# Kernel optimization log

Measured on AMD Instinct MI355X. Metric: run time of the kernel, lower is better.

The kernel has to match this reference:

```python
import jax, jax.numpy as jnp
import numpy as np

N_NODES = 50000
N_EDGES = 600000
IN_CH = 128
OUT_CH = 128


def setup_inputs() -> dict:
    key = jax.random.key(0)
    k1, k2, k3, k4 = jax.random.split(key, 4)
    x = jax.random.normal(k1, (N_NODES, IN_CH), dtype=jnp.float32)
    edge_index = jax.random.randint(k2, (2, N_EDGES), 0, N_NODES, dtype=jnp.int64)
    W_msg = jax.random.normal(k3, (OUT_CH, IN_CH * 9), dtype=jnp.float32) * (1.0 / np.sqrt(IN_CH * 9))
    b_msg = jnp.zeros((OUT_CH,), dtype=jnp.float32)
    W_root = jax.random.normal(k4, (OUT_CH, IN_CH), dtype=jnp.float32) * (1.0 / np.sqrt(IN_CH))
    b_root = jnp.zeros((OUT_CH,), dtype=jnp.float32)
    return {"x": x, "edge_index": edge_index, "W_msg": W_msg, "b_msg": b_msg,
            "W_root": W_root, "b_root": b_root}


def reference(x, edge_index, W_msg, b_msg, W_root, b_root):
    n = x.shape[0]
    src = edge_index[0]
    dst = edge_index[1]

    # in-degree per destination node
    degree = jax.ops.segment_sum(jnp.ones_like(dst, dtype=x.dtype), dst, num_segments=n)  # [N]

    msgs = x[src]  # [E, C] gathered source features
    agg_sum = jax.ops.segment_sum(msgs, dst, num_segments=n)                 # [N, C]
    agg_mean = agg_sum / jnp.maximum(degree, 1.0)[:, None]                    # [N, C]
    agg_max = jax.ops.segment_max(msgs, dst, num_segments=n)                  # [N, C], -inf for empty
    agg_max = jnp.where(degree[:, None] > 0, agg_max, 0.0)

    degree_term = jnp.log1p(degree + 1.0)[:, None]                            # [N, 1]
    degree_reference = jnp.maximum(jnp.mean(jnp.log1p(degree + 1.0)), 1.0)    # scalar

    amp = degree_term / degree_reference                                       # [N, 1]
    att = degree_reference / jnp.maximum(degree_term, 1e-06)                   # [N, 1]

    feats = []
    for agg in (agg_sum, agg_mean, agg_max):
        feats.append(agg)            # identity
        feats.append(agg * amp)      # amplification
        feats.append(agg * att)      # attenuation
    stacked = jnp.concatenate(feats, axis=-1)                                  # [N, 9C]

    return stacked @ W_msg.T + b_msg + x @ W_root.T + b_root
```

## Files before the change

### kernel.cpp

```cpp
#include <hip/hip_runtime.h>
#include <cmath>

#define IN_CH 128
#define OUT_CH 128
#define KDIM 512
#define NGEMM 384
#define GBM 256
#define GBN 192
#define SLOT_B 40960
#define SLOT_US 20480
#define PIPE_LDS_BYTES (3 * SLOT_B)

typedef __attribute__((ext_vector_type(8))) short bfrag;
typedef __attribute__((ext_vector_type(4))) float f32x4;

__device__ __forceinline__ unsigned short f2bf(float f) {
    unsigned int u = __float_as_uint(f);
    return (unsigned short)((u + 0x7FFFu + ((u >> 16) & 1u)) >> 16);
}
__device__ __forceinline__ float bf2f(unsigned short h) {
    return __uint_as_float(((unsigned int)h) << 16);
}
__device__ __forceinline__ float4 unpack4(uint2 u) {
    float4 r;
    r.x = __uint_as_float(u.x << 16);
    r.y = __uint_as_float(u.x & 0xFFFF0000u);
    r.z = __uint_as_float(u.y << 16);
    r.w = __uint_as_float(u.y & 0xFFFF0000u);
    return r;
}

__device__ __forceinline__ void gl2lds16(const void* g, void* l) {
    __builtin_amdgcn_global_load_lds(
        (const __attribute__((address_space(1))) unsigned int*)g,
        (__attribute__((address_space(3))) unsigned int*)l, 16, 0, 0);
}


__global__ __launch_bounds__(256) void prep_kernel(const int* __restrict__ ei,
                                                   int* __restrict__ degree,
                                                   float* __restrict__ logsum,
                                                   const float* __restrict__ x,
                                                   unsigned short* __restrict__ xb,
                                                   int E, int total4) {
    int i = blockIdx.x * 256 + threadIdx.x;
    if (i == 0) logsum[0] = 0.f;
    if (i < E) atomicAdd(&degree[ei[E + i]], 1);
    if (i < total4) {
        float4 v = ((const float4*)x)[i];
        uint2 p;
        p.x = (unsigned)f2bf(v.x) | ((unsigned)f2bf(v.y) << 16);
        p.y = (unsigned)f2bf(v.z) | ((unsigned)f2bf(v.w) << 16);
        ((uint2*)xb)[i] = p;
    }
}

__global__ __launch_bounds__(256) void scan1_kernel(const int* __restrict__ degree,
                                                    int* __restrict__ part,
                                                    float* __restrict__ logsum, int n) {
    int i = blockIdx.x * 256 + threadIdx.x;
    int d = (i < n) ? degree[i] : 0;
    float lg = (i < n) ? logf((float)d + 2.0f) : 0.f;
    #pragma unroll
    for (int off = 32; off; off >>= 1) {
        d += __shfl_down(d, off);
        lg += __shfl_down(lg, off);
    }
    __shared__ int sd[4];
    __shared__ float sl[4];
    int wv = threadIdx.x >> 6;
    if ((threadIdx.x & 63) == 0) { sd[wv] = d; sl[wv] = lg; }
    __syncthreads();
    if (threadIdx.x == 0) {
        part[blockIdx.x] = (sd[0] + sd[1]) + (sd[2] + sd[3]);
        atomicAdd(&logsum[0], (sl[0] + sl[1]) + (sl[2] + sl[3]));
    }
}

__global__ __launch_bounds__(256) void scan3_kernel(const int* __restrict__ degree,
                                                    const int* __restrict__ part,
                                                    int* __restrict__ offsets,
                                                    int n, int E, int Sb) {
    int tid = threadIdx.x;
    int i = blockIdx.x * 256 + tid;
    int b = blockIdx.x;
    int acc0 = 0;
    for (int j = tid; j < b; j += 256) acc0 += part[j];
    #pragma unroll
    for (int off = 32; off; off >>= 1) acc0 += __shfl_down(acc0, off);
    __shared__ int bsum[4];
    int lane = tid & 63, wv = tid >> 6;
    if (lane == 0) bsum[wv] = acc0;
    __syncthreads();
    int base = (bsum[0] + bsum[1]) + (bsum[2] + bsum[3]);

    int d = (i < n) ? degree[i] : 0;
    int s = d;
    #pragma unroll
    for (int off = 1; off < 64; off <<= 1) {
        int t = __shfl_up(s, off);
        if (lane >= off) s += t;
    }
    __shared__ int wsum[4];
    if (lane == 63) wsum[wv] = s;
    __syncthreads();
    for (int w2 = 0; w2 < wv; ++w2) base += wsum[w2];
    if (i < n) offsets[i] = base + s - d;
    if (i == n - 1) offsets[n] = E;
}

__global__ void fill_kernel(const int* __restrict__ ei, int* __restrict__ offsets,
                            int* __restrict__ csr_src, int E) {
    int e = blockIdx.x * blockDim.x + threadIdx.x;
    if (e < E) {
        int src = ei[e];
        int dst = ei[E + e];
        int pos = atomicAdd(&offsets[dst], 1);
        csr_src[pos] = src;
    }
}


__global__ __launch_bounds__(256) void agg_kernel(const unsigned short* __restrict__ xb,
                                                  const int* __restrict__ csr_src,
                                                  const int* __restrict__ offsets,
                                                  const int* __restrict__ degree,
                                                  const float* __restrict__ logsum,
                                                  unsigned short* __restrict__ Zhi,
                                                  float* __restrict__ ampv,
                                                  float* __restrict__ attv,
                                                  int N, int Mpad) {
    int node = (blockIdx.x * 256 + threadIdx.x) >> 6;
    int lane = threadIdx.x & 63;
    if (node >= Mpad) return;
    int h = lane >> 5;
    int c4 = lane & 31;
    long zbase = (long)node * KDIM + c4 * 4;
    if (node >= N) {
        if (h == 0) {
            uint2 z = make_uint2(0u, 0u);
            #pragma unroll
            for (int sec = 0; sec < 4; ++sec) *(uint2*)&Zhi[zbase + sec * 128] = z;
        }
        return;
    }
    int deg = degree[node];
    int end = offsets[node];
    int beg = end - deg;
    const float NEG = -3.402823466e38f;
    float4 s[4], m[4];
    #pragma unroll
    for (int u = 0; u < 4; ++u) {
        s[u] = make_float4(0.f, 0.f, 0.f, 0.f);
        m[u] = make_float4(NEG, NEG, NEG, NEG);
    }
    int i = beg;
    for (; i + 8 <= end; i += 8) {
        int idx[4];
        #pragma unroll
        for (int u = 0; u < 4; ++u) idx[u] = csr_src[i + u * 2 + h];
        uint2 raw[4];
        #pragma unroll
        for (int u = 0; u < 4; ++u) raw[u] = *(const uint2*)&xb[(long)idx[u] * IN_CH + c4 * 4];
        #pragma unroll
        for (int u = 0; u < 4; ++u) {
            float4 v = unpack4(raw[u]);
            s[u].x += v.x; s[u].y += v.y; s[u].z += v.z; s[u].w += v.w;
            m[u].x = fmaxf(m[u].x, v.x); m[u].y = fmaxf(m[u].y, v.y);
            m[u].z = fmaxf(m[u].z, v.z); m[u].w = fmaxf(m[u].w, v.w);
        }
    }
    for (; i < end; i += 2) {
        int e = i + h;
        if (e < end) {
            float4 v = unpack4(*(const uint2*)&xb[(long)csr_src[e] * IN_CH + c4 * 4]);
            s[0].x += v.x; s[0].y += v.y; s[0].z += v.z; s[0].w += v.w;
            m[0].x = fmaxf(m[0].x, v.x); m[0].y = fmaxf(m[0].y, v.y);
            m[0].z = fmaxf(m[0].z, v.z); m[0].w = fmaxf(m[0].w, v.w);
        }
    }
    float4 sum, mx;
    sum.x = (s[0].x + s[1].x) + (s[2].x + s[3].x);
    sum.y = (s[0].y + s[1].y) + (s[2].y + s[3].y);
    sum.z = (s[0].z + s[1].z) + (s[2].z + s[3].z);
    sum.w = (s[0].w + s[1].w) + (s[2].w + s[3].w);
    mx.x = fmaxf(fmaxf(m[0].x, m[1].x), fmaxf(m[2].x, m[3].x));
    mx.y = fmaxf(fmaxf(m[0].y, m[1].y), fmaxf(m[2].y, m[3].y));
    mx.z = fmaxf(fmaxf(m[0].z, m[1].z), fmaxf(m[2].z, m[3].z));
    mx.w = fmaxf(fmaxf(m[0].w, m[1].w), fmaxf(m[2].w, m[3].w));
    sum.x += __shfl_xor(sum.x, 32); sum.y += __shfl_xor(sum.y, 32);
    sum.z += __shfl_xor(sum.z, 32); sum.w += __shfl_xor(sum.w, 32);
    mx.x = fmaxf(mx.x, __shfl_xor(mx.x, 32)); mx.y = fmaxf(mx.y, __shfl_xor(mx.y, 32));
    mx.z = fmaxf(mx.z, __shfl_xor(mx.z, 32)); mx.w = fmaxf(mx.w, __shfl_xor(mx.w, 32));

    float inv = 1.0f / fmaxf((float)deg, 1.0f);
    float4 mean = make_float4(sum.x * inv, sum.y * inv, sum.z * inv, sum.w * inv);
    if (deg == 0) mx = make_float4(0.f, 0.f, 0.f, 0.f);
    float4 xv = unpack4(*(const uint2*)&xb[(long)node * IN_CH + c4 * 4]);

    if (h == 0) {
        float4 secs[4] = { xv, sum, mean, mx };
        #pragma unroll
        for (int sec = 0; sec < 4; ++sec) {
            float4 v = secs[sec];
            uint2 hi;
            hi.x = (unsigned)f2bf(v.x) | ((unsigned)f2bf(v.y) << 16);
            hi.y = (unsigned)f2bf(v.z) | ((unsigned)f2bf(v.w) << 16);
            *(uint2*)&Zhi[zbase + sec * 128] = hi;
        }
    }
    if (lane == 0) {
        float ref = fmaxf(logsum[0] / (float)N, 1.0f);
        float dt = log1pf((float)deg + 1.0f);
        ampv[node] = dt / ref;
        attv[node] = ref / fmaxf(dt, 1e-6f);
    }
}


__global__ void wbuild_kernel(const float* __restrict__ Wmsg, const float* __restrict__ Wroot,
                              unsigned short* __restrict__ Whi, unsigned short* __restrict__ Wlo) {
    int idx = blockIdx.x * 256 + threadIdx.x;
    if (idx >= NGEMM * KDIM) return;
    int jp = idx >> 9;
    int k = idx & 511;
    int cg = jp / 96;
    int rem = jp - cg * 96;
    int s16 = rem >> 4;
    int r16 = rem & 15;
    int wn2 = s16 / 3;
    int sec = s16 - wn2 * 3;
    int ocol = cg * 32 + wn2 * 16 + r16;
    float v;
    if (k < 128) {
        v = (sec == 0) ? Wroot[ocol * 128 + k] : 0.f;
    } else {
        int a = (k - 128) >> 7;
        int c = (k - 128) & 127;
        v = Wmsg[ocol * 1152 + (a * 3 + sec) * 128 + c];
    }
    unsigned short h = f2bf(v);
    Whi[idx] = h;
    Wlo[idx] = f2bf(v - bf2f(h));
}


__global__ __launch_bounds__(1024, 4) void gemm_pipe(const unsigned short* __restrict__ Zhi,
                                                     const unsigned short* __restrict__ Whi,
                                                     const unsigned short* __restrict__ Wlo,
                                                     const float* __restrict__ ampv,
                                                     const float* __restrict__ attv,
                                                     const float* __restrict__ bmsg,
                                                     const float* __restrict__ broot,
                                                     float* __restrict__ out, int M) {
    extern __shared__ char smem[];
    unsigned short* lds = (unsigned short*)smem;
    const int tid = threadIdx.x;
    const int w = tid >> 6;
    const int lane = tid & 63;
    const int r16 = lane & 15, q = lane >> 4;
    const int wm = w >> 2, wn = w & 3;
    const int row0 = blockIdx.x * GBM;
    const int cg2 = blockIdx.y;

    const unsigned short* sAh = Zhi + (long)(row0 + w * 16 + r16) * KDIM + q * 8;
    const unsigned short* sB2 = (w < 12)
        ? Whi + (long)(cg2 * GBN + w * 16 + r16) * KDIM + q * 8
        : Wlo + (long)(cg2 * GBN + (w - 12) * 16 + r16) * KDIM + q * 8;
    const unsigned short* sB3 = Wlo + (long)(cg2 * GBN + (4 + w) * 16 + r16) * KDIM + q * 8;
    const int d0 = tid * 16, d2 = (1024 + tid) * 16, d3 = (2048 + tid) * 16;

    gl2lds16(sAh, smem + d0); gl2lds16(sB2, smem + d2); if (w < 8) gl2lds16(sB3, smem + d3);
    sAh += 32; sB2 += 32; sB3 += 32;
    gl2lds16(sAh, smem + SLOT_B + d0); gl2lds16(sB2, smem + SLOT_B + d2);
    if (w < 8) gl2lds16(sB3, smem + SLOT_B + d3);
    sAh += 32; sB2 += 32; sB3 += 32;

    if (w < 8) __builtin_amdgcn_s_waitcnt(0x0F73);
    else       __builtin_amdgcn_s_waitcnt(0x0F72);
    __builtin_amdgcn_s_barrier();
    __builtin_amdgcn_sched_barrier(0);

    f32x4 acc[4][3] = {};
    const int jtb = (wn >> 1) * 6 + (wn & 1) * 3;

    #pragma unroll 1
    for (int it = 0; it < 4; ++it) {
        const int s = it % 3;
        {
            char* b = smem + ((it + 2) % 3) * SLOT_B;
            gl2lds16(sAh, b + d0); gl2lds16(sB2, b + d2); if (w < 8) gl2lds16(sB3, b + d3);
            sAh += 32; sB2 += 32; sB3 += 32;
        }
        const unsigned short* L = lds + s * SLOT_US;

        int chb = jtb * 512 + lane * 8;
        bfrag bh0 = *(const bfrag*)&L[8192 + chb];
        bfrag bl0 = *(const bfrag*)&L[14336 + chb];
        #pragma unroll
        for (int mt = 0; mt < 4; ++mt) {
            bfrag ah = *(const bfrag*)&L[((wm * 4 + mt) * 64 + lane) * 8];
            acc[mt][0] = __builtin_amdgcn_mfma_f32_16x16x32_bf16(ah, bh0, acc[mt][0], 0, 0, 0);
            acc[mt][0] = __builtin_amdgcn_mfma_f32_16x16x32_bf16(ah, bl0, acc[mt][0], 0, 0, 0);
        }

        if (w < 8) __builtin_amdgcn_s_waitcnt(0x0F73);
        else       __builtin_amdgcn_s_waitcnt(0x0F72);
        __builtin_amdgcn_s_barrier();
        __builtin_amdgcn_sched_barrier(0);
    }

    #pragma unroll 1
    for (int it = 4; it < 16; ++it) {
        const int s = it % 3;
        if (it + 2 < 16) {
            char* b = smem + ((it + 2) % 3) * SLOT_B;
            gl2lds16(sAh, b + d0); gl2lds16(sB2, b + d2); if (w < 8) gl2lds16(sB3, b + d3);
            sAh += 32; sB2 += 32; sB3 += 32;
        }
        const unsigned short* L = lds + s * SLOT_US;

        bfrag bh[3], bl[3];
        #pragma unroll
        for (int nt = 0; nt < 3; ++nt) {
            int chb = (jtb + nt) * 512 + lane * 8;
            bh[nt] = *(const bfrag*)&L[8192 + chb];
            bl[nt] = *(const bfrag*)&L[14336 + chb];
        }
        #pragma unroll
        for (int mt = 0; mt < 4; ++mt) {
            bfrag ah = *(const bfrag*)&L[((wm * 4 + mt) * 64 + lane) * 8];
            #pragma unroll
            for (int nt = 0; nt < 3; ++nt) {
                acc[mt][nt] = __builtin_amdgcn_mfma_f32_16x16x32_bf16(ah, bh[nt], acc[mt][nt], 0, 0, 0);
                acc[mt][nt] = __builtin_amdgcn_mfma_f32_16x16x32_bf16(ah, bl[nt], acc[mt][nt], 0, 0, 0);
            }
        }

        if (it < 14) {
            if (w < 8) __builtin_amdgcn_s_waitcnt(0x0F73);
            else       __builtin_amdgcn_s_waitcnt(0x0F72);
        } else if (it == 14) {
            __builtin_amdgcn_s_waitcnt(0x0F70);
        }
        if (it < 15) {
            __builtin_amdgcn_s_barrier();
            __builtin_amdgcn_sched_barrier(0);
        }
    }

    const int col = (cg2 * 2 + (wn >> 1)) * 32 + (wn & 1) * 16 + r16;
    const float bias = bmsg[col] + broot[col];
    #pragma unroll
    for (int mt = 0; mt < 4; ++mt) {
        #pragma unroll
        for (int r = 0; r < 4; ++r) {
            int row = row0 + wm * 64 + mt * 16 + q * 4 + r;
            if (row < M) {
                float v = acc[mt][0][r]
                        + ampv[row] * acc[mt][1][r]
                        + attv[row] * acc[mt][2][r] + bias;
                out[(long)row * OUT_CH + col] = v;
            }
        }
    }
}


__global__ __launch_bounds__(1024, 4) void gemm_sb(const unsigned short* __restrict__ Zhi,
                                                   const unsigned short* __restrict__ Whi,
                                                   const unsigned short* __restrict__ Wlo,
                                                   const float* __restrict__ ampv,
                                                   const float* __restrict__ attv,
                                                   const float* __restrict__ bmsg,
                                                   const float* __restrict__ broot,
                                                   float* __restrict__ out, int M) {
    __shared__ unsigned short lds[SLOT_US];
    const int tid = threadIdx.x;
    const int w = tid >> 6;
    const int lane = tid & 63;
    const int r16 = lane & 15, q = lane >> 4;
    const int wm = w >> 2, wn = w & 3;
    const int row0 = blockIdx.x * GBM;
    const int cg2 = blockIdx.y;

    const unsigned short* sAh = Zhi + (long)(row0 + w * 16 + r16) * KDIM + q * 8;
    const unsigned short* sB2 = (w < 12)
        ? Whi + (long)(cg2 * GBN + w * 16 + r16) * KDIM + q * 8
        : Wlo + (long)(cg2 * GBN + (w - 12) * 16 + r16) * KDIM + q * 8;
    const unsigned short* sB3 = Wlo + (long)(cg2 * GBN + (4 + w) * 16 + r16) * KDIM + q * 8;
    char* ldsb = (char*)lds;
    const int d0 = tid * 16, d2 = (1024 + tid) * 16, d3 = (2048 + tid) * 16;

    f32x4 acc[4][3] = {};
    const int jtb = (wn >> 1) * 6 + (wn & 1) * 3;

    #pragma unroll 1
    for (int it = 0; it < 16; ++it) {
        if (it) __syncthreads();
        gl2lds16(sAh, ldsb + d0); gl2lds16(sB2, ldsb + d2); if (w < 8) gl2lds16(sB3, ldsb + d3);
        sAh += 32; sB2 += 32; sB3 += 32;
        __syncthreads();

        bfrag bh[3], bl[3];
        #pragma unroll
        for (int nt = 0; nt < 3; ++nt) {
            int chb = (jtb + nt) * 512 + lane * 8;
            bh[nt] = *(const bfrag*)&lds[8192 + chb];
            bl[nt] = *(const bfrag*)&lds[14336 + chb];
        }
        #pragma unroll
        for (int mt = 0; mt < 4; ++mt) {
            bfrag ah = *(const bfrag*)&lds[((wm * 4 + mt) * 64 + lane) * 8];
            #pragma unroll
            for (int nt = 0; nt < 3; ++nt) {
                acc[mt][nt] = __builtin_amdgcn_mfma_f32_16x16x32_bf16(ah, bh[nt], acc[mt][nt], 0, 0, 0);
                acc[mt][nt] = __builtin_amdgcn_mfma_f32_16x16x32_bf16(ah, bl[nt], acc[mt][nt], 0, 0, 0);
            }
        }
    }

    const int col = (cg2 * 2 + (wn >> 1)) * 32 + (wn & 1) * 16 + r16;
    const float bias = bmsg[col] + broot[col];
    #pragma unroll
    for (int mt = 0; mt < 4; ++mt) {
        #pragma unroll
        for (int r = 0; r < 4; ++r) {
            int row = row0 + wm * 64 + mt * 16 + q * 4 + r;
            if (row < M) {
                float v = acc[mt][0][r]
                        + ampv[row] * acc[mt][1][r]
                        + attv[row] * acc[mt][2][r] + bias;
                out[(long)row * OUT_CH + col] = v;
            }
        }
    }
}


extern "C" void kernel_launch(void* const* d_in, const int* in_sizes, int n_in,
                              void* d_out, int out_size, void* d_ws, size_t ws_size,
                              hipStream_t stream) {
    const float* x     = (const float*)d_in[0];
    const int*   ei    = (const int*)d_in[1];
    const float* Wmsg  = (const float*)d_in[2];
    const float* bmsg  = (const float*)d_in[3];
    const float* Wroot = (const float*)d_in[4];
    const float* broot = (const float*)d_in[5];
    float* out = (float*)d_out;

    int N = in_sizes[0] / IN_CH;
    int E = in_sizes[1] / 2;
    int Mb = (N + GBM - 1) / GBM;
    int Mpad = Mb * GBM;
    int Sb = (N + 255) / 256;
    int total4 = N * IN_CH / 4;

    char* ws = (char*)d_ws;
    size_t off = 0;
    auto alloc = [&](size_t bytes) -> void* {
        void* p = ws + off;
        off = (off + bytes + 255) & ~(size_t)255;
        return p;
    };
    int* degree  = (int*)alloc((size_t)N * 4);
    int* offsets = (int*)alloc((size_t)(N + 1) * 4);
    float* logsum = (float*)alloc(4);
    int* part    = (int*)alloc((size_t)Sb * 4);
    int* csr_src = (int*)alloc((size_t)E * 4);
    unsigned short* Whi = (unsigned short*)alloc((size_t)NGEMM * KDIM * 2);
    unsigned short* Wlo = (unsigned short*)alloc((size_t)NGEMM * KDIM * 2);
    unsigned short* Zhi = (unsigned short*)alloc((size_t)Mpad * KDIM * 2);
    unsigned short* xb  = (unsigned short*)alloc((size_t)Mpad * IN_CH * 2);
    float* ampv = (float*)alloc((size_t)N * 4);
    float* attv = (float*)alloc((size_t)N * 4);

    hipMemsetAsync(degree, 0, (size_t)N * 4, stream);

    int prepg = (max(E, total4) + 255) / 256;
    prep_kernel<<<prepg, 256, 0, stream>>>(ei, degree, logsum, x, xb, E, total4);
    scan1_kernel<<<Sb, 256, 0, stream>>>(degree, part, logsum, N);
    scan3_kernel<<<Sb, 256, 0, stream>>>(degree, part, offsets, N, E, Sb);
    fill_kernel<<<(E + 255) / 256, 256, 0, stream>>>(ei, offsets, csr_src, E);
    agg_kernel<<<(Mpad * 64 + 255) / 256, 256, 0, stream>>>(xb, csr_src, offsets, degree, logsum,
                                                            Zhi, ampv, attv, N, Mpad);
    wbuild_kernel<<<(NGEMM * KDIM + 255) / 256, 256, 0, stream>>>(Wmsg, Wroot, Whi, Wlo);

    bool pipe = false;
    int dev = 0;
    if (hipGetDevice(&dev) == hipSuccess) {
        int optin = 0;
        if (hipDeviceGetAttribute(&optin, hipDeviceAttributeSharedMemPerBlockOptin, dev) == hipSuccess
            && optin >= (int)PIPE_LDS_BYTES) {
            pipe = (hipFuncSetAttribute((const void*)gemm_pipe,
                                        hipFuncAttributeMaxDynamicSharedMemorySize,
                                        PIPE_LDS_BYTES) == hipSuccess);
        }
    }
    dim3 ggrid(Mb, 2);
    if (pipe) {
        gemm_pipe<<<ggrid, 1024, PIPE_LDS_BYTES, stream>>>(Zhi, Whi, Wlo, ampv, attv,
                                                           bmsg, broot, out, N);
    } else {
        gemm_sb<<<ggrid, 1024, 0, stream>>>(Zhi, Whi, Wlo, ampv, attv,
                                            bmsg, broot, out, N);
    }
}
```

Baseline: 242.7 us.

## Enlarge pipelined GEMM row tile to 384 and rebalance LDS loads across waves

The pipelined GEMM kernel now processes 384 rows per block instead of 256, giving each wave 6 M-subtiles and a larger accumulator array. The global-to-LDS staging is redistributed so every wave issues exactly three 16-byte loads per stage. This removes the uneven wait counts and the separate warm-up loop that skipped the amp and att columns for the first K-steps. Each B fragment is reused across more rows, which lowers LDS and global traffic per output, at the cost of more registers, a 144KB LDS footprint and fewer blocks in flight (padding goes to 768).

```diff
diff --git a/kernel.cpp b/kernel.cpp
--- a/kernel.cpp
+++ b/kernel.cpp
@@ -6,9 +6,11 @@
 #define KDIM 512
 #define NGEMM 384
 #define GBM 256
+#define GBMP 384
 #define GBN 192
-#define SLOT_B 40960
-#define SLOT_US 20480
+#define SLOT_B 49152
+#define SLOT_US 24576
+#define SB_SLOT_US 20480
 #define PIPE_LDS_BYTES (3 * SLOT_B)
 
 typedef __attribute__((ext_vector_type(8))) short bfrag;
@@ -260,63 +262,45 @@
     const int lane = tid & 63;
     const int r16 = lane & 15, q = lane >> 4;
     const int wm = w >> 2, wn = w & 3;
-    const int row0 = blockIdx.x * GBM;
+    const int row0 = blockIdx.x * GBMP;
     const int cg2 = blockIdx.y;
 
-    const unsigned short* sAh = Zhi + (long)(row0 + w * 16 + r16) * KDIM + q * 8;
-    const unsigned short* sB2 = (w < 12)
-        ? Whi + (long)(cg2 * GBN + w * 16 + r16) * KDIM + q * 8
-        : Wlo + (long)(cg2 * GBN + (w - 12) * 16 + r16) * KDIM + q * 8;
-    const unsigned short* sB3 = Wlo + (long)(cg2 * GBN + (4 + w) * 16 + r16) * KDIM + q * 8;
-    const int d0 = tid * 16, d2 = (1024 + tid) * 16, d3 = (2048 + tid) * 16;
-
-    gl2lds16(sAh, smem + d0); gl2lds16(sB2, smem + d2); if (w < 8) gl2lds16(sB3, smem + d3);
-    sAh += 32; sB2 += 32; sB3 += 32;
-    gl2lds16(sAh, smem + SLOT_B + d0); gl2lds16(sB2, smem + SLOT_B + d2);
-    if (w < 8) gl2lds16(sB3, smem + SLOT_B + d3);
-    sAh += 32; sB2 += 32; sB3 += 32;
-
-    if (w < 8) __builtin_amdgcn_s_waitcnt(0x0F73);
-    else       __builtin_amdgcn_s_waitcnt(0x0F72);
+    const unsigned short* sP0;
+    int dd0;
+    if (w < 8) {
+        sP0 = Zhi + (long)(row0 + (3 * w) * 16 + r16) * KDIM + q * 8;
+        dd0 = (3 * w) * 1024 + lane * 16;
+    } else {
+        const int c0 = 3 * (w - 8);
+        const unsigned short* Wb = (w < 12) ? Whi : Wlo;
+        const int rr = (w < 12) ? c0 * 16 : (c0 - 12) * 16;
+        sP0 = Wb + (long)(cg2 * GBN + rr + r16) * KDIM + q * 8;
+        dd0 = 24576 + c0 * 1024 + lane * 16;
+    }
+    const unsigned short* sP1 = sP0 + 16 * KDIM;
+    const unsigned short* sP2 = sP0 + 32 * KDIM;
+    const int dd1 = dd0 + 1024, dd2 = dd0 + 2048;
+
+    gl2lds16(sP0, smem + dd0); gl2lds16(sP1, smem + dd1); gl2lds16(sP2, smem + dd2);
+    sP0 += 32; sP1 += 32; sP2 += 32;
+    gl2lds16(sP0, smem + SLOT_B + dd0); gl2lds16(sP1, smem + SLOT_B + dd1);
+    gl2lds16(sP2, smem + SLOT_B + dd2);
+    sP0 += 32; sP1 += 32; sP2 += 32;
+
+    __builtin_amdgcn_s_waitcnt(0x0F73);
     __builtin_amdgcn_s_barrier();
     __builtin_amdgcn_sched_barrier(0);
 
-    f32x4 acc[4][3] = {};
+    f32x4 acc[6][3] = {};
     const int jtb = (wn >> 1) * 6 + (wn & 1) * 3;
 
     #pragma unroll 1
-    for (int it = 0; it < 4; ++it) {
-        const int s = it % 3;
-        {
-            char* b = smem + ((it + 2) % 3) * SLOT_B;
-            gl2lds16(sAh, b + d0); gl2lds16(sB2, b + d2); if (w < 8) gl2lds16(sB3, b + d3);
-            sAh += 32; sB2 += 32; sB3 += 32;
-        }
-        const unsigned short* L = lds + s * SLOT_US;
-
-        int chb = jtb * 512 + lane * 8;
-        bfrag bh0 = *(const bfrag*)&L[8192 + chb];
-        bfrag bl0 = *(const bfrag*)&L[14336 + chb];
-        #pragma unroll
-        for (int mt = 0; mt < 4; ++mt) {
-            bfrag ah = *(const bfrag*)&L[((wm * 4 + mt) * 64 + lane) * 8];
-            acc[mt][0] = __builtin_amdgcn_mfma_f32_16x16x32_bf16(ah, bh0, acc[mt][0], 0, 0, 0);
-            acc[mt][0] = __builtin_amdgcn_mfma_f32_16x16x32_bf16(ah, bl0, acc[mt][0], 0, 0, 0);
-        }
-
-        if (w < 8) __builtin_amdgcn_s_waitcnt(0x0F73);
-        else       __builtin_amdgcn_s_waitcnt(0x0F72);
-        __builtin_amdgcn_s_barrier();
-        __builtin_amdgcn_sched_barrier(0);
-    }
-
-    #pragma unroll 1
-    for (int it = 4; it < 16; ++it) {
+    for (int it = 0; it < 16; ++it) {
         const int s = it % 3;
         if (it + 2 < 16) {
             char* b = smem + ((it + 2) % 3) * SLOT_B;
-            gl2lds16(sAh, b + d0); gl2lds16(sB2, b + d2); if (w < 8) gl2lds16(sB3, b + d3);
-            sAh += 32; sB2 += 32; sB3 += 32;
+            gl2lds16(sP0, b + dd0); gl2lds16(sP1, b + dd1); gl2lds16(sP2, b + dd2);
+            sP0 += 32; sP1 += 32; sP2 += 32;
         }
         const unsigned short* L = lds + s * SLOT_US;
 
@@ -324,12 +308,12 @@
         #pragma unroll
         for (int nt = 0; nt < 3; ++nt) {
             int chb = (jtb + nt) * 512 + lane * 8;
-            bh[nt] = *(const bfrag*)&L[8192 + chb];
-            bl[nt] = *(const bfrag*)&L[14336 + chb];
-        }
-        #pragma unroll
-        for (int mt = 0; mt < 4; ++mt) {
-            bfrag ah = *(const bfrag*)&L[((wm * 4 + mt) * 64 + lane) * 8];
+            bh[nt] = *(const bfrag*)&L[12288 + chb];
+            bl[nt] = *(const bfrag*)&L[18432 + chb];
+        }
+        #pragma unroll
+        for (int mt = 0; mt < 6; ++mt) {
+            bfrag ah = *(const bfrag*)&L[((wm * 6 + mt) * 64 + lane) * 8];
             #pragma unroll
             for (int nt = 0; nt < 3; ++nt) {
                 acc[mt][nt] = __builtin_amdgcn_mfma_f32_16x16x32_bf16(ah, bh[nt], acc[mt][nt], 0, 0, 0);
@@ -337,12 +321,8 @@
             }
         }
 
-        if (it < 14) {
-            if (w < 8) __builtin_amdgcn_s_waitcnt(0x0F73);
-            else       __builtin_amdgcn_s_waitcnt(0x0F72);
-        } else if (it == 14) {
-            __builtin_amdgcn_s_waitcnt(0x0F70);
-        }
+        if (it < 14)       __builtin_amdgcn_s_waitcnt(0x0F73);
+        else if (it == 14) __builtin_amdgcn_s_waitcnt(0x0F70);
         if (it < 15) {
             __builtin_amdgcn_s_barrier();
             __builtin_amdgcn_sched_barrier(0);
@@ -352,10 +332,10 @@
     const int col = (cg2 * 2 + (wn >> 1)) * 32 + (wn & 1) * 16 + r16;
     const float bias = bmsg[col] + broot[col];
     #pragma unroll
-    for (int mt = 0; mt < 4; ++mt) {
+    for (int mt = 0; mt < 6; ++mt) {
         #pragma unroll
         for (int r = 0; r < 4; ++r) {
-            int row = row0 + wm * 64 + mt * 16 + q * 4 + r;
+            int row = row0 + wm * 96 + mt * 16 + q * 4 + r;
             if (row < M) {
                 float v = acc[mt][0][r]
                         + ampv[row] * acc[mt][1][r]
@@ -375,7 +355,7 @@
                                                    const float* __restrict__ bmsg,
                                                    const float* __restrict__ broot,
                                                    float* __restrict__ out, int M) {
-    __shared__ unsigned short lds[SLOT_US];
+    __shared__ unsigned short lds[SB_SLOT_US];
     const int tid = threadIdx.x;
     const int w = tid >> 6;
     const int lane = tid & 63;
@@ -451,8 +431,10 @@
 
     int N = in_sizes[0] / IN_CH;
     int E = in_sizes[1] / 2;
-    int Mb = (N + GBM - 1) / GBM;
-    int Mpad = Mb * GBM;
+    int Mb768 = (N + 767) / 768;
+    int Mpad = Mb768 * 768;
+    int MbP = Mpad / GBMP;
+    int MbS = Mpad / GBM;
     int Sb = (N + 255) / 256;
     int total4 = N * IN_CH / 4;
 
@@ -497,11 +479,12 @@
                                         PIPE_LDS_BYTES) == hipSuccess);
         }
     }
-    dim3 ggrid(Mb, 2);
     if (pipe) {
+        dim3 ggrid(MbP, 2);
         gemm_pipe<<<ggrid, 1024, PIPE_LDS_BYTES, stream>>>(Zhi, Whi, Wlo, ampv, attv,
                                                            bmsg, broot, out, N);
     } else {
+        dim3 ggrid(MbS, 2);
         gemm_sb<<<ggrid, 1024, 0, stream>>>(Zhi, Whi, Wlo, ampv, attv,
                                             bmsg, broot, out, N);
     }
```

Measured after the change: 258.0 us. 1.06x slower.
